# Kernel tuning notes

Hardware: AMD Instinct MI355X
Metric: run time of the kernel (lower is better)

Reference implementation:

```python
import jax, jax.numpy as jnp
import numpy as np

B = 32768
E = 10  # number of motion experts


def _p(k, shape, scale=0.05):
    return jax.random.normal(k, shape, dtype=jnp.float32) * scale


def setup_inputs() -> dict:
    key = jax.random.key(0)
    ks = jax.random.split(key, 24)
    inp = {"input_": jax.random.normal(ks[0], (B, 556), dtype=jnp.float32)}
    # encoder 0: pose 400 -> 512 -> 512
    inp["e0_W0"] = _p(ks[1], (400, 512)); inp["e0_b0"] = jnp.zeros((512,), jnp.float32)
    inp["e0_W1"] = _p(ks[2], (512, 512)); inp["e0_b1"] = jnp.zeros((512,), jnp.float32)
    # encoder 1: goal 78 -> 128 -> 128
    inp["e1_W0"] = _p(ks[3], (78, 128)); inp["e1_b0"] = jnp.zeros((128,), jnp.float32)
    inp["e1_W1"] = _p(ks[4], (128, 128)); inp["e1_b1"] = jnp.zeros((128,), jnp.float32)
    # gating NN (1 expert => plain MLP): 78 -> 512 -> 512 -> 10, softmax
    inp["g_W0"] = _p(ks[5], (78, 512)); inp["g_b0"] = jnp.zeros((512,), jnp.float32)
    inp["g_W1"] = _p(ks[6], (512, 512)); inp["g_b1"] = jnp.zeros((512,), jnp.float32)
    inp["g_W2"] = _p(ks[7], (512, 10)); inp["g_b2"] = jnp.zeros((10,), jnp.float32)
    # motion prediction ComponentNN: 10 experts, 640 -> 512 -> 512 -> 578
    inp["m_W0"] = _p(ks[8], (E, 640, 512)); inp["m_b0"] = jnp.zeros((E, 512), jnp.float32)
    inp["m_W1"] = _p(ks[9], (E, 512, 512)); inp["m_b1"] = jnp.zeros((E, 512), jnp.float32)
    inp["m_W2"] = _p(ks[10], (E, 512, 578)); inp["m_b2"] = jnp.zeros((E, 578), jnp.float32)
    return inp


def _expert_layer(x, w, W, b):
    # sum_e w[b,e] * (x[b] @ W[e] + b[e]); blend outputs (equiv. to blending weights)
    return jnp.einsum('be,bi,eio->bo', w, x, W) + w @ b


def reference(input_, e0_W0, e0_b0, e0_W1, e0_b1, e1_W0, e1_b0, e1_W1, e1_b1,
              g_W0, g_b0, g_W1, g_b1, g_W2, g_b2,
              m_W0, m_b0, m_W1, m_b1, m_W2, m_b2):
    elu = jax.nn.elu
    pose = input_[:, 0:400]
    goal = input_[:, 400:478]
    gate_in = input_[:, 478:556]
    # encoders (dropout inactive at inference)
    h0 = elu(elu(pose @ e0_W0 + e0_b0) @ e0_W1 + e0_b1)   # [B,512]
    h1 = elu(elu(goal @ e1_W0 + e1_b0) @ e1_W1 + e1_b1)   # [B,128]
    # gating: softmax over 10 experts
    g = elu(gate_in @ g_W0 + g_b0)
    g = elu(g @ g_W1 + g_b1)
    w = jax.nn.softmax(g @ g_W2 + g_b2, axis=-1)          # [B,10]
    feat = jnp.concatenate([h0, h1], axis=-1)             # [B,640]
    x = elu(_expert_layer(feat, w, m_W0, m_b0))
    x = elu(_expert_layer(x, w, m_W1, m_b1))
    pred = _expert_layer(x, w, m_W2, m_b2)                # [B,578], linear final
    return pred
```

## Files before the change

kernel.cpp:

```cpp
#include <hip/hip_runtime.h>
#include <math.h>

typedef _Float16 h8 __attribute__((ext_vector_type(8)));
typedef float f4 __attribute__((ext_vector_type(4)));

#define BATCH 32768

__device__ __forceinline__ void gload16(const void* g, void* l) {
  __builtin_amdgcn_global_load_lds(
      (const __attribute__((address_space(1))) unsigned int*)g,
      (__attribute__((address_space(3))) unsigned int*)l, 16, 0, 0);
}

__global__ __launch_bounds__(256) void prep_input2_k(const float* __restrict__ in,
    _Float16* __restrict__ pose, _Float16* __restrict__ goal, _Float16* __restrict__ gate)
{
  const long long total = (long long)BATCH * 88;
  for (long long i = (long long)blockIdx.x * 256 + threadIdx.x; i < total;
       i += (long long)gridDim.x * 256) {
    const int b = (int)(i / 88);
    const int g = (int)(i % 88);
    const float* r = in + (size_t)b * 556;
    h8 v;
    if (g < 56) {
      const int c0 = g * 8;
      #pragma unroll
      for (int j = 0; j < 8; ++j) {
        const int c = c0 + j;
        v[j] = (_Float16)((c < 400) ? r[c] : (c == 400 ? 1.0f : 0.0f));
      }
      *reinterpret_cast<h8*>(pose + (size_t)b * 448 + c0) = v;
    } else if (g < 72) {
      const int c0 = (g - 56) * 8;
      #pragma unroll
      for (int j = 0; j < 8; ++j) {
        const int c = c0 + j;
        v[j] = (_Float16)((c < 78) ? r[400 + c] : (c == 78 ? 1.0f : 0.0f));
      }
      *reinterpret_cast<h8*>(goal + (size_t)b * 128 + c0) = v;
    } else {
      const int c0 = (g - 72) * 8;
      #pragma unroll
      for (int j = 0; j < 8; ++j) {
        const int c = c0 + j;
        v[j] = (_Float16)((c < 78) ? r[478 + c] : (c == 78 ? 1.0f : 0.0f));
      }
      *reinterpret_cast<h8*>(gate + (size_t)b * 128 + c0) = v;
    }
  }
}

__global__ __launch_bounds__(256) void prep_wt_k(const float* __restrict__ W,
    const float* __restrict__ bias, _Float16* __restrict__ out,
    int K, int N, int Nld, int Kout, int biasCols, int biasLd)
{
  __shared__ float tile[64 * 65];
  const int t = threadIdx.x;
  const int c0 = blockIdx.x * 64;
  const int n0 = blockIdx.y * 64;
  {
    const int nn = t & 63;
    #pragma unroll
    for (int i = 0; i < 16; ++i) {
      int cc = (t >> 6) + i * 4;
      int c = c0 + cc, n = n0 + nn;
      float v = 0.0f;
      if (n < N) {
        if (c < K) v = W[(size_t)c * Nld + n];
        else if (c - K < biasCols) v = bias[(size_t)(c - K) * biasLd + n];
      }
      tile[cc * 65 + nn] = v;
    }
  }
  __syncthreads();
  {
    const int cc = t & 63;
    #pragma unroll
    for (int i = 0; i < 16; ++i) {
      int nn = (t >> 6) + i * 4;
      out[(size_t)(n0 + nn) * Kout + c0 + cc] = (_Float16)tile[cc * 65 + nn];
    }
  }
}

template<bool EPI_BIAS, bool DO_ELU, bool OUT_F32>
__global__ __launch_bounds__(256, 2) void gemm_k(
    const _Float16* __restrict__ A, const _Float16* __restrict__ Bw,
    void* __restrict__ OutP, const float* __restrict__ bias,
    int ldA, int ldB, int ldO, int nChunks, int nLimit)
{
  __shared__ __align__(16) _Float16 As[2][128 * 64];
  __shared__ __align__(16) _Float16 Bs[2][128 * 64];

  const int t = threadIdx.x;
  const int m0 = blockIdx.x * 128;
  const int n0 = blockIdx.y * 128;
  const int wid = t >> 6;
  const int lane = t & 63;
  const int wm = (wid >> 1) * 64;
  const int wn = (wid & 1) * 64;
  const int lr = lane & 15;
  const int lg = lane >> 4;

  const int gr = lane >> 3;
  const int gcol = ((lane & 7) ^ gr) * 8;
  const _Float16* Abase = A + (size_t)(m0 + wid * 32 + gr) * ldA + gcol;
  const _Float16* Bbase = Bw + (size_t)(n0 + wid * 32 + gr) * ldB + gcol;

  f4 acc[4][4];
  #pragma unroll
  for (int i = 0; i < 4; ++i)
    #pragma unroll
    for (int j = 0; j < 4; ++j) { f4 z = {0.f, 0.f, 0.f, 0.f}; acc[i][j] = z; }

  auto issue = [&](int c, int buf) {
    #pragma unroll
    for (int i = 0; i < 4; ++i) {
      gload16(Abase + (size_t)(i * 8) * ldA + c * 64, &As[buf][(wid * 32 + i * 8) * 64]);
      gload16(Bbase + (size_t)(i * 8) * ldB + c * 64, &Bs[buf][(wid * 32 + i * 8) * 64]);
    }
  };

  auto mfma_step = [&](const _Float16* as, const _Float16* bs) {
    #pragma unroll
    for (int kk = 0; kk < 2; ++kk) {
      h8 af[4], bf[4];
      const int kslot = kk * 4 + lg;
      #pragma unroll
      for (int i = 0; i < 4; ++i) {
        const int row = wm + i * 16 + lr;
        af[i] = *reinterpret_cast<const h8*>(&as[row * 64 + ((kslot ^ (row & 7)) << 3)]);
      }
      #pragma unroll
      for (int j = 0; j < 4; ++j) {
        const int row = wn + j * 16 + lr;
        bf[j] = *reinterpret_cast<const h8*>(&bs[row * 64 + ((kslot ^ (row & 7)) << 3)]);
      }
      #pragma unroll
      for (int i = 0; i < 4; ++i)
        #pragma unroll
        for (int j = 0; j < 4; ++j)
          acc[i][j] = __builtin_amdgcn_mfma_f32_16x16x32_f16(af[i], bf[j], acc[i][j], 0, 0, 0);
    }
  };

  issue(0, 0);
  int cur = 0;
  for (int c = 0; c < nChunks; ++c) {
    __syncthreads();
    if (c + 1 < nChunks) issue(c + 1, cur ^ 1);
    mfma_step(As[cur], Bs[cur]);
    cur ^= 1;
  }

  #pragma unroll
  for (int j = 0; j < 4; ++j) {
    const int col = n0 + wn + j * 16 + lr;
    if (col >= nLimit) continue;
    float bvv = 0.0f;
    if (EPI_BIAS) bvv = bias[col];
    #pragma unroll
    for (int i = 0; i < 4; ++i) {
      const int rowb = m0 + wm + i * 16 + lg * 4;
      #pragma unroll
      for (int r = 0; r < 4; ++r) {
        float x = acc[i][j][r] + bvv;
        if (DO_ELU) x = (x > 0.0f) ? x : expm1f(x);
        if (OUT_F32)
          reinterpret_cast<float*>(OutP)[(size_t)(rowb + r) * ldO + col] = x;
        else
          reinterpret_cast<_Float16*>(OutP)[(size_t)(rowb + r) * ldO + col] = (_Float16)x;
      }
    }
  }
}

template<int KCe, int NI, bool DO_ELU, bool OUT_F32>
__global__ __launch_bounds__(256, 2) void expertV_k(
    const _Float16* __restrict__ A, const _Float16* __restrict__ Bw,
    void* __restrict__ OutP, const _Float16* __restrict__ wpad,
    int ldA, int ldB, int ldO, int nLimit)
{
  constexpr int E = 10;
  constexpr int S = KCe * E + 1;
  constexpr int SG = NI / 2;
  constexpr int SLOT = NI * 1024;
  __shared__ __align__(16) _Float16 lds[3 * SLOT + 2560];
  _Float16* wT = lds + 3 * SLOT;

  const int tid = threadIdx.x;
  const int w = tid >> 6;
  const int l = tid & 63;
  const int m0 = blockIdx.x * 256;
  const int n0 = blockIdx.y * (NI * 16);
  const int lr = l & 15;
  const int lg = l >> 4;

  const int strow = tid >> 3;
  const int scol = ((tid & 7) ^ (strow & 7)) * 8;

  auto stB = [&](int slot, size_t colEl) {
    _Float16* d = lds + slot * SLOT + w * 512;
    const _Float16* sp = Bw + (size_t)(n0 + strow) * ldB + colEl + scol;
    #pragma unroll
    for (int p = 0; p < SG; ++p)
      gload16(sp + (size_t)(p * 32) * ldB, d + p * 2048);
  };

  auto frag = [&](const _Float16* base, int row, int kslot) -> h8 {
    return *reinterpret_cast<const h8*>(base + row * 64 + ((kslot ^ (row & 7)) << 3));
  };

  h8 araw[2][4];
  auto loadA = [&](const _Float16* base, size_t ld, size_t col0) {
    #pragma unroll
    for (int kk = 0; kk < 2; ++kk)
      #pragma unroll
      for (int mi = 0; mi < 4; ++mi)
        araw[kk][mi] = *reinterpret_cast<const h8*>(
            base + (size_t)(m0 + w * 64 + mi * 16 + lr) * ld + col0 + (size_t)(kk * 4 + lg) * 8);
  };

  f4 acc[4][NI];
  #pragma unroll
  for (int mi = 0; mi < 4; ++mi)
    #pragma unroll
    for (int ni = 0; ni < NI; ++ni) { f4 z = {0.f, 0.f, 0.f, 0.f}; acc[mi][ni] = z; }

  #pragma unroll
  for (int idx = tid; idx < 2560; idx += 256) {
    const int m = idx & 255, e = idx >> 8;
    wT[e * 256 + m] = wpad[(size_t)(m0 + m) * 64 + e];
  }
  loadA(A, (size_t)ldA, 0);
  stB(0, 0);
  stB(1, (size_t)KCe * 64);
  if constexpr (SG == 4) asm volatile("s_waitcnt vmcnt(4)" ::: "memory");
  else                   asm volatile("s_waitcnt vmcnt(5)" ::: "memory");
  asm volatile("s_waitcnt lgkmcnt(0)" ::: "memory");
  __builtin_amdgcn_s_barrier();
  __builtin_amdgcn_sched_barrier(0);

  int e_s = 0, kc_s = 0;
  int e_t = 2, kc_t = 0;
  #pragma unroll 1
  for (int s = 0; s < S; ++s) {
    const _Float16* Bh = lds + (s % 3) * SLOT;

    if (s + 2 < S) {
      const size_t col = (kc_t < KCe) ? (size_t)(e_t * KCe + kc_t) * 64
                                      : (size_t)(E * KCe) * 64;
      stB((s + 2) % 3, col);
    }
    __builtin_amdgcn_sched_barrier(0);

    const bool isBias = (kc_s == KCe);
    _Float16 se[4];
    if (!isBias) {
      #pragma unroll
      for (int j = 0; j < 4; ++j) se[j] = wT[e_s * 256 + w * 64 + j * 16 + lr];
    }

    #pragma unroll
    for (int kk = 0; kk < 2; ++kk) {
      h8 aa[4];
      #pragma unroll
      for (int mi = 0; mi < 4; ++mi) {
        h8 v = araw[kk][mi];
        if (!isBias) {
          const _Float16 sv = se[mi];
          #pragma unroll
          for (int q = 0; q < 8; ++q) v[q] = v[q] * sv;
        }
        aa[mi] = v;
      }
      #pragma unroll
      for (int c0 = 0; c0 < NI; c0 += 4) {
        h8 bf[4];
        #pragma unroll
        for (int ni = 0; ni < 4; ++ni)
          if (c0 + ni < NI) bf[ni] = frag(Bh, (c0 + ni) * 16 + lr, kk * 4 + lg);
        __builtin_amdgcn_s_setprio(1);
        #pragma unroll
        for (int mi = 0; mi < 4; ++mi)
          #pragma unroll
          for (int ni = 0; ni < 4; ++ni)
            if (c0 + ni < NI)
              acc[mi][c0 + ni] =
                  __builtin_amdgcn_mfma_f32_16x16x32_f16(aa[mi], bf[ni], acc[mi][c0 + ni], 0, 0, 0);
        __builtin_amdgcn_s_setprio(0);
      }
    }
    __builtin_amdgcn_sched_barrier(0);

    if (s + 1 < S) {
      if (s + 2 < S) {
        if constexpr (SG == 4) asm volatile("s_waitcnt vmcnt(4)" ::: "memory");
        else                   asm volatile("s_waitcnt vmcnt(5)" ::: "memory");
      } else {
        asm volatile("s_waitcnt vmcnt(0)" ::: "memory");
      }
      __builtin_amdgcn_s_barrier();
      __builtin_amdgcn_sched_barrier(0);
      if (e_s == E - 1) {
        if (kc_s + 1 < KCe) loadA(A, (size_t)ldA, (size_t)(kc_s + 1) * 64);
        else                loadA(wpad, 64, 0);
        e_s = 0; ++kc_s;
      } else ++e_s;
      if (kc_t < KCe) { if (e_t == E - 1) { e_t = 0; ++kc_t; } else ++e_t; }
    }
  }

  #pragma unroll
  for (int ni = 0; ni < NI; ++ni) {
    const int col = n0 + ni * 16 + lr;
    if (col >= nLimit) continue;
    #pragma unroll
    for (int mi = 0; mi < 4; ++mi) {
      const int rowb = m0 + w * 64 + mi * 16 + lg * 4;
      #pragma unroll
      for (int r = 0; r < 4; ++r) {
        float x = acc[mi][ni][r];
        if (DO_ELU) x = (x > 0.0f) ? x : expm1f(x);
        if (OUT_F32)
          reinterpret_cast<float*>(OutP)[(size_t)(rowb + r) * ldO + col] = x;
        else
          reinterpret_cast<_Float16*>(OutP)[(size_t)(rowb + r) * ldO + col] = (_Float16)x;
      }
    }
  }
}

__global__ __launch_bounds__(256) void gate_softmax_k(const _Float16* __restrict__ gb,
    const float* __restrict__ W2, const float* __restrict__ b2, _Float16* __restrict__ wpad)
{
  __shared__ float W2s[5120];
  for (int i = threadIdx.x; i < 5120; i += 256) W2s[i] = W2[i];
  __syncthreads();
  const int t = threadIdx.x;
  const int sub = t & 3;
  const int b = blockIdx.x * 64 + (t >> 2);
  const _Float16* row = gb + (size_t)b * 512 + sub * 128;
  float acc[10];
  #pragma unroll
  for (int o = 0; o < 10; ++o) acc[o] = 0.0f;
  #pragma unroll 4
  for (int k0 = 0; k0 < 128; k0 += 8) {
    h8 x = *reinterpret_cast<const h8*>(row + k0);
    #pragma unroll
    for (int jj = 0; jj < 8; ++jj) {
      float xv = (float)x[jj];
      const int k = sub * 128 + k0 + jj;
      #pragma unroll
      for (int o = 0; o < 10; ++o) acc[o] += xv * W2s[k * 10 + o];
    }
  }
  #pragma unroll
  for (int o = 0; o < 10; ++o) {
    acc[o] += __shfl_xor(acc[o], 1);
    acc[o] += __shfl_xor(acc[o], 2);
    acc[o] += b2[o];
  }
  float mx = acc[0];
  #pragma unroll
  for (int o = 1; o < 10; ++o) mx = fmaxf(mx, acc[o]);
  float s = 0.0f;
  #pragma unroll
  for (int o = 0; o < 10; ++o) { acc[o] = expf(acc[o] - mx); s += acc[o]; }
  const float inv = 1.0f / s;
  h8 o0 = {0,0,0,0,0,0,0,0}, o1 = {0,0,0,0,0,0,0,0};
  if (sub == 0) {
    #pragma unroll
    for (int o = 0; o < 8; ++o) o0[o] = (_Float16)(acc[o] * inv);
    o1[0] = (_Float16)(acc[8] * inv);
    o1[1] = (_Float16)(acc[9] * inv);
  }
  _Float16* wr = wpad + (size_t)b * 64 + sub * 16;
  *reinterpret_cast<h8*>(wr) = o0;
  *reinterpret_cast<h8*>(wr + 8) = o1;
}

extern "C" void kernel_launch(void* const* d_in, const int* in_sizes, int n_in,
                              void* d_out, int out_size, void* d_ws, size_t ws_size,
                              hipStream_t stream)
{
  const float* input_ = (const float*)d_in[0];
  const float* e0_W0 = (const float*)d_in[1];
  const float* e0_b0 = (const float*)d_in[2];
  const float* e0_W1 = (const float*)d_in[3];
  const float* e0_b1 = (const float*)d_in[4];
  const float* e1_W0 = (const float*)d_in[5];
  const float* e1_b0 = (const float*)d_in[6];
  const float* e1_W1 = (const float*)d_in[7];
  const float* e1_b1 = (const float*)d_in[8];
  const float* g_W0  = (const float*)d_in[9];
  const float* g_b0  = (const float*)d_in[10];
  const float* g_W1  = (const float*)d_in[11];
  const float* g_b1  = (const float*)d_in[12];
  const float* g_W2  = (const float*)d_in[13];
  const float* g_b2  = (const float*)d_in[14];
  const float* m_W0  = (const float*)d_in[15];
  const float* m_b0  = (const float*)d_in[16];
  const float* m_W1  = (const float*)d_in[17];
  const float* m_b1  = (const float*)d_in[18];
  const float* m_W2  = (const float*)d_in[19];
  const float* m_b2  = (const float*)d_in[20];
  (void)in_sizes; (void)n_in; (void)out_size; (void)ws_size;

  char* ws = (char*)d_ws;
  size_t off = 0;
  auto alloc = [&](size_t bytes) { char* p = ws + off; off += (bytes + 255) & ~(size_t)255; return p; };

  const size_t Bn = BATCH;
  _Float16* wsA    = (_Float16*)alloc(Bn * 512 * 2);
  _Float16* wsB    = (_Float16*)alloc(Bn * 512 * 2);
  _Float16* wsC    = (_Float16*)alloc(Bn * 640 * 2);
  _Float16* goal16 = (_Float16*)alloc(Bn * 128 * 2);
  _Float16* gate16 = (_Float16*)alloc(Bn * 128 * 2);
  _Float16* h1a16  = (_Float16*)alloc(Bn * 128 * 2);
  _Float16* wpad16 = (_Float16*)alloc(Bn * 64 * 2);
  _Float16* e0W0t  = (_Float16*)alloc((size_t)512 * 448 * 2);
  _Float16* e0W1t  = (_Float16*)alloc((size_t)512 * 512 * 2);
  _Float16* e1W0t  = (_Float16*)alloc((size_t)128 * 128 * 2);
  _Float16* e1W1t  = (_Float16*)alloc((size_t)128 * 128 * 2);
  _Float16* gW0t   = (_Float16*)alloc((size_t)512 * 128 * 2);
  _Float16* gW1t   = (_Float16*)alloc((size_t)512 * 512 * 2);
  _Float16* W0b    = (_Float16*)alloc((size_t)512 * 6464 * 2);
  _Float16* W1b    = (_Float16*)alloc((size_t)512 * 5184 * 2);
  _Float16* W2b    = (_Float16*)alloc((size_t)768 * 5184 * 2);

  dim3 blk(256);
  const int BIG = 1 << 30;

  prep_input2_k<<<dim3(2048), blk, 0, stream>>>(input_, wsA, goal16, gate16);

  prep_wt_k<<<dim3(7, 8),    blk, 0, stream>>>(e0_W0, e0_b0, e0W0t, 400, 512, 512, 448, 1, 0);
  prep_wt_k<<<dim3(8, 8),    blk, 0, stream>>>(e0_W1, nullptr, e0W1t, 512, 512, 512, 512, 0, 0);
  prep_wt_k<<<dim3(2, 2),    blk, 0, stream>>>(e1_W0, e1_b0, e1W0t, 78, 128, 128, 128, 1, 0);
  prep_wt_k<<<dim3(2, 2),    blk, 0, stream>>>(e1_W1, nullptr, e1W1t, 128, 128, 128, 128, 0, 0);
  prep_wt_k<<<dim3(2, 8),    blk, 0, stream>>>(g_W0, g_b0, gW0t, 78, 512, 512, 128, 1, 0);
  prep_wt_k<<<dim3(8, 8),    blk, 0, stream>>>(g_W1, nullptr, gW1t, 512, 512, 512, 512, 0, 0);
  prep_wt_k<<<dim3(101, 8),  blk, 0, stream>>>(m_W0, m_b0, W0b, 6400, 512, 512, 6464, 10, 512);
  prep_wt_k<<<dim3(81, 8),   blk, 0, stream>>>(m_W1, m_b1, W1b, 5120, 512, 512, 5184, 10, 512);
  prep_wt_k<<<dim3(81, 12),  blk, 0, stream>>>(m_W2, m_b2, W2b, 5120, 578, 578, 5184, 10, 578);

  gemm_k<false, true, false><<<dim3(256, 4), blk, 0, stream>>>(
      wsA, e0W0t, wsB, nullptr, 448, 448, 512, 7, BIG);
  gemm_k<true, true, false><<<dim3(256, 4), blk, 0, stream>>>(
      wsB, e0W1t, wsC, e0_b1, 512, 512, 640, 8, BIG);
  gemm_k<false, true, false><<<dim3(256, 1), blk, 0, stream>>>(
      goal16, e1W0t, h1a16, nullptr, 128, 128, 128, 2, BIG);
  gemm_k<true, true, false><<<dim3(256, 1), blk, 0, stream>>>(
      h1a16, e1W1t, wsC + 512, e1_b1, 128, 128, 640, 2, BIG);
  gemm_k<false, true, false><<<dim3(256, 4), blk, 0, stream>>>(
      gate16, gW0t, wsA, nullptr, 128, 128, 512, 2, BIG);
  gemm_k<true, true, false><<<dim3(256, 4), blk, 0, stream>>>(
      wsA, gW1t, wsB, g_b1, 512, 512, 512, 8, BIG);
  gate_softmax_k<<<dim3(BATCH / 64), blk, 0, stream>>>(wsB, g_W2, g_b2, wpad16);

  expertV_k<10, 8, true, false><<<dim3(128, 4), blk, 0, stream>>>(
      wsC, W0b, wsA, wpad16, 640, 6464, 512, BIG);
  expertV_k<8, 8, true, false><<<dim3(128, 4), blk, 0, stream>>>(
      wsA, W1b, wsC, wpad16, 512, 5184, 512, BIG);
  expertV_k<8, 10, false, true><<<dim3(128, 4), blk, 0, stream>>>(
      wsC, W2b, d_out, wpad16, 512, 5184, 578, 578);
}
```

Measured before the change: 861.8 us.

## Add register-resident A expert GEMM kernel with per-expert scaling for first two layers

Introduces expertH_k, which keeps the activation tile in registers and scales it by each row's gate weight per expert on the fly. Only the expert weight tiles are streamed through double-buffered, XOR-swizzled LDS, and the bias is folded in through a final pass over wpad. The kernel uses 128x128 tiles with 4 blocks per CU instead of the previous larger-M tiles, and replaces expertV_k for layers 0 and 1. In exchange it adds per-element fp16 multiplies in the inner loop and reloads the B tile for every expert and chunk.

Measured after the change: 875.1 us. About the same (+1.5%).

```diff
diff --git a/kernel.cpp b/kernel.cpp
--- a/kernel.cpp
+++ b/kernel.cpp
@@ -165,6 +165,160 @@
       #pragma unroll
       for (int r = 0; r < 4; ++r) {
         float x = acc[i][j][r] + bvv;
+        if (DO_ELU) x = (x > 0.0f) ? x : expm1f(x);
+        if (OUT_F32)
+          reinterpret_cast<float*>(OutP)[(size_t)(rowb + r) * ldO + col] = x;
+        else
+          reinterpret_cast<_Float16*>(OutP)[(size_t)(rowb + r) * ldO + col] = (_Float16)x;
+      }
+    }
+  }
+}
+
+template<int KCe, bool DO_ELU, bool OUT_F32>
+__global__ __launch_bounds__(256, 4) void expertH_k(
+    const _Float16* __restrict__ A, const _Float16* __restrict__ Bw,
+    void* __restrict__ OutP, const _Float16* __restrict__ wpad,
+    int ldA, int ldB, int ldO, int nLimit)
+{
+  constexpr int E = 10;
+  __shared__ __align__(16) _Float16 lds[16384 + 1280];
+  _Float16* Bs = lds;
+  _Float16* wT = lds + 16384;
+
+  const int tid = threadIdx.x;
+  const int w = tid >> 6;
+  const int l = tid & 63;
+  const int m0 = blockIdx.x * 128;
+  const int n0 = blockIdx.y * 128;
+  const int lr = l & 15;
+  const int lg = l >> 4;
+
+  const int strow = tid >> 3;
+  const int scol = ((tid & 7) ^ (strow & 7)) * 8;
+
+  auto stB = [&](int buf, size_t colEl) {
+    _Float16* d = Bs + buf * 8192 + w * 512;
+    const _Float16* s = Bw + (size_t)(n0 + strow) * ldB + colEl + scol;
+    #pragma unroll
+    for (int p = 0; p < 4; ++p)
+      gload16(s + (size_t)(p * 32) * ldB, d + p * 2048);
+  };
+
+  auto frag = [&](const _Float16* base, int row, int kslot) -> h8 {
+    return *reinterpret_cast<const h8*>(base + row * 64 + ((kslot ^ (row & 7)) << 3));
+  };
+
+  h8 araw[2][2];
+  auto loadA = [&](const _Float16* base, size_t ld, size_t col0) {
+    #pragma unroll
+    for (int kk = 0; kk < 2; ++kk)
+      #pragma unroll
+      for (int mi = 0; mi < 2; ++mi)
+        araw[kk][mi] = *reinterpret_cast<const h8*>(
+            base + (size_t)(m0 + w * 32 + mi * 16 + lr) * ld + col0 + (size_t)(kk * 4 + lg) * 8);
+  };
+
+  f4 acc[2][8];
+  #pragma unroll
+  for (int mi = 0; mi < 2; ++mi)
+    #pragma unroll
+    for (int ni = 0; ni < 8; ++ni) { f4 z = {0.f, 0.f, 0.f, 0.f}; acc[mi][ni] = z; }
+
+  #pragma unroll
+  for (int idx = tid; idx < 1280; idx += 256) {
+    const int m = idx & 127, e = idx >> 7;
+    wT[e * 128 + m] = wpad[(size_t)(m0 + m) * 64 + e];
+  }
+  loadA(A, (size_t)ldA, 0);
+  stB(0, 0);
+  asm volatile("s_waitcnt vmcnt(0) lgkmcnt(0)" ::: "memory");
+  __builtin_amdgcn_s_barrier();
+  __builtin_amdgcn_sched_barrier(0);
+
+  int s = 0;
+  #pragma unroll 1
+  for (int kc = 0; kc < KCe; ++kc) {
+    #pragma unroll 1
+    for (int e = 0; e < E; ++e, ++s) {
+      const _Float16* Bh = Bs + (s & 1) * 8192;
+
+      if (e + 1 < E)         stB((s + 1) & 1, (size_t)((e + 1) * KCe + kc) * 64);
+      else if (kc + 1 < KCe) stB((s + 1) & 1, (size_t)(kc + 1) * 64);
+      else                   stB((s + 1) & 1, (size_t)(E * KCe) * 64);
+      __builtin_amdgcn_sched_barrier(0);
+
+      _Float16 se[2];
+      #pragma unroll
+      for (int j = 0; j < 2; ++j) se[j] = wT[e * 128 + w * 32 + j * 16 + lr];
+
+      #pragma unroll
+      for (int kk = 0; kk < 2; ++kk) {
+        h8 aa[2];
+        #pragma unroll
+        for (int mi = 0; mi < 2; ++mi) {
+          h8 v = araw[kk][mi];
+          const _Float16 sv = se[mi];
+          #pragma unroll
+          for (int q = 0; q < 8; ++q) v[q] = v[q] * sv;
+          aa[mi] = v;
+        }
+        #pragma unroll
+        for (int c0 = 0; c0 < 8; c0 += 4) {
+          h8 bf[4];
+          #pragma unroll
+          for (int ni = 0; ni < 4; ++ni)
+            bf[ni] = frag(Bh, (c0 + ni) * 16 + lr, kk * 4 + lg);
+          __builtin_amdgcn_s_setprio(1);
+          #pragma unroll
+          for (int mi = 0; mi < 2; ++mi)
+            #pragma unroll
+            for (int ni = 0; ni < 4; ++ni)
+              acc[mi][c0 + ni] =
+                  __builtin_amdgcn_mfma_f32_16x16x32_f16(aa[mi], bf[ni], acc[mi][c0 + ni], 0, 0, 0);
+          __builtin_amdgcn_s_setprio(0);
+        }
+      }
+
+      __builtin_amdgcn_sched_barrier(0);
+      asm volatile("s_waitcnt vmcnt(0)" ::: "memory");
+      __builtin_amdgcn_s_barrier();
+      __builtin_amdgcn_sched_barrier(0);
+    }
+    if (kc + 1 < KCe) loadA(A, (size_t)ldA, (size_t)(kc + 1) * 64);
+    else              loadA(wpad, 64, 0);
+  }
+
+  {
+    const _Float16* Bh = Bs + (s & 1) * 8192;
+    #pragma unroll
+    for (int kk = 0; kk < 2; ++kk) {
+      #pragma unroll
+      for (int c0 = 0; c0 < 8; c0 += 4) {
+        h8 bf[4];
+        #pragma unroll
+        for (int ni = 0; ni < 4; ++ni)
+          bf[ni] = frag(Bh, (c0 + ni) * 16 + lr, kk * 4 + lg);
+        #pragma unroll
+        for (int mi = 0; mi < 2; ++mi)
+          #pragma unroll
+          for (int ni = 0; ni < 4; ++ni)
+            acc[mi][c0 + ni] =
+                __builtin_amdgcn_mfma_f32_16x16x32_f16(araw[kk][mi], bf[ni], acc[mi][c0 + ni], 0, 0, 0);
+      }
+    }
+  }
+
+  #pragma unroll
+  for (int ni = 0; ni < 8; ++ni) {
+    const int col = n0 + ni * 16 + lr;
+    if (col >= nLimit) continue;
+    #pragma unroll
+    for (int mi = 0; mi < 2; ++mi) {
+      const int rowb = m0 + w * 32 + mi * 16 + lg * 4;
+      #pragma unroll
+      for (int r = 0; r < 4; ++r) {
+        float x = acc[mi][ni][r];
         if (DO_ELU) x = (x > 0.0f) ? x : expm1f(x);
         if (OUT_F32)
           reinterpret_cast<float*>(OutP)[(size_t)(rowb + r) * ldO + col] = x;
@@ -458,9 +612,9 @@
       wsA, gW1t, wsB, g_b1, 512, 512, 512, 8, BIG);
   gate_softmax_k<<<dim3(BATCH / 64), blk, 0, stream>>>(wsB, g_W2, g_b2, wpad16);
 
-  expertV_k<10, 8, true, false><<<dim3(128, 4), blk, 0, stream>>>(
+  expertH_k<10, true, false><<<dim3(256, 4), blk, 0, stream>>>(
       wsC, W0b, wsA, wpad16, 640, 6464, 512, BIG);
-  expertV_k<8, 8, true, false><<<dim3(128, 4), blk, 0, stream>>>(
+  expertH_k<8, true, false><<<dim3(256, 4), blk, 0, stream>>>(
       wsA, W1b, wsC, wpad16, 512, 5184, 512, BIG);
   expertV_k<8, 10, false, true><<<dim3(128, 4), blk, 0, stream>>>(
       wsC, W2b, d_out, wpad16, 512, 5184, 578, 578);
```
